# Kernel tuning notes

Measured on AMD Instinct MI355X. Metric: run time of the kernel, lower is better.

Reference implementation:

```python
import jax, jax.numpy as jnp
import numpy as np


def setup_inputs() -> dict:
    key = jax.random.key(0)
    ks = jax.random.split(key, 4)
    B, T, M, E, F = 4, 2048, 1024, 8, 4096
    hidden_states = jax.random.normal(ks[0], (B, T, M), dtype=jnp.float32)
    wg = jax.random.normal(ks[1], (M, E), dtype=jnp.float32) * (1.0 / np.sqrt(M))
    w1 = jax.random.normal(ks[2], (E, M, F), dtype=jnp.float32) * (1.0 / np.sqrt(M))
    b1 = jnp.zeros((E, F), dtype=jnp.float32)
    w2 = jax.random.normal(ks[3], (E, F, M), dtype=jnp.float32) * (1.0 / np.sqrt(F))
    b2 = jnp.zeros((E, M), dtype=jnp.float32)
    return {"hidden_states": hidden_states, "wg": wg, "w1": w1, "b1": b1, "w2": w2, "b2": b2}


def reference(hidden_states, wg, w1, b1, w2, b2):
    B, T, M = hidden_states.shape
    E = wg.shape[1]
    S = B * T
    MIN_CAPACITY = 4
    C = max((S + E - 1) // E, MIN_CAPACITY)  # capacity_factor = 1 (static)

    x = hidden_states.reshape(S, M)  # [S, M]

    # --- top-1 gating (deepspeed TopKGate, noisy=None, use_rts=False) ---
    logits = x @ wg                                  # [S, E]
    gates = jax.nn.softmax(logits, axis=-1)          # [S, E]
    idx = jnp.argmax(gates, axis=-1)                 # [S]
    mask1 = jax.nn.one_hot(idx, E, dtype=gates.dtype)  # [S, E]
    # aux loss (computed before capacity drop)
    l_aux = jnp.sum(gates.mean(0) * mask1.mean(0)) * E
    # position of each token within its expert's queue
    locations1 = jnp.cumsum(mask1, axis=0) - 1.0     # [S, E]
    mask1 = mask1 * (locations1 < C)                 # drop overflow tokens
    gates1_s = jnp.sum(gates * mask1, axis=1)        # [S]
    loc_s = jnp.sum(locations1 * mask1, axis=1).astype(jnp.int32)  # [S]
    loc_sc = jax.nn.one_hot(loc_s, C, dtype=gates.dtype)           # [S, C]

    combine_weights = jnp.einsum('se,sc->sec', gates1_s[:, None] * mask1, loc_sc)  # [S,E,C]
    dispatch_mask = (combine_weights > 0).astype(x.dtype)

    # --- dispatch ---
    dispatched = jnp.einsum('sec,sm->ecm', dispatch_mask, x)  # [E, C, M]

    # --- expert FFN (grouped GEMM) ---
    h = jax.nn.gelu(jnp.einsum('ecm,emf->ecf', dispatched, w1) + b1[:, None, :])
    expert_out = jnp.einsum('ecf,efm->ecm', h, w2) + b2[:, None, :]  # [E, C, M]

    # --- combine ---
    out = jnp.einsum('sec,ecm->sm', combine_weights, expert_out)  # [S, M]
    return out.reshape(B, T, M)
```

## Files before the change

kernel.cpp:

```cpp
#include <hip/hip_runtime.h>
#include <hip/hip_bf16.h>
#include <math.h>

#define S_TOK 8192
#define M_DIM 1024
#define E_NUM 8
#define F_DIM 4096
#define CAP   1024

typedef short short8 __attribute__((ext_vector_type(8)));
typedef float f32x4 __attribute__((ext_vector_type(4)));
typedef unsigned short ushortx4 __attribute__((ext_vector_type(4)));

__device__ inline unsigned short f2bf(float f) {
    union { float f; unsigned int u; } v; v.f = f;
    unsigned int r = v.u + 0x7fffu + ((v.u >> 16) & 1u);
    return (unsigned short)(r >> 16);
}

__device__ inline float gelu_fast(float x) {
    float y = 0.7978845608028654f * (x + 0.044715f * x * x * x);
    if (y > 40.f) return x;
    float e = exp2f(2.8853900817779268f * y);
    return x * e / (e + 1.0f);
}

__device__ inline void gl_lds16(const void* g, void* l) {
    __builtin_amdgcn_global_load_lds(
        (const __attribute__((address_space(1))) unsigned int*)g,
        (__attribute__((address_space(3))) unsigned int*)l, 16, 0, 0);
}

__global__ __launch_bounds__(256) void gating_kernel(
    const float* __restrict__ x, const float* __restrict__ wg,
    int* __restrict__ idx, float* __restrict__ gate)
{
    int wid = threadIdx.x >> 6;
    int lane = threadIdx.x & 63;
    int s = blockIdx.x * 4 + wid;
    const float* xs = x + (size_t)s * M_DIM;

    double acc[E_NUM];
#pragma unroll
    for (int e = 0; e < E_NUM; e++) acc[e] = 0.0;

    for (int i = lane; i < M_DIM; i += 64) {
        float xv = xs[i];
        float4 wa = *(const float4*)(wg + (size_t)i * E_NUM);
        float4 wb = *(const float4*)(wg + (size_t)i * E_NUM + 4);
        acc[0] += (double)xv * (double)wa.x;
        acc[1] += (double)xv * (double)wa.y;
        acc[2] += (double)xv * (double)wa.z;
        acc[3] += (double)xv * (double)wa.w;
        acc[4] += (double)xv * (double)wb.x;
        acc[5] += (double)xv * (double)wb.y;
        acc[6] += (double)xv * (double)wb.z;
        acc[7] += (double)xv * (double)wb.w;
    }
#pragma unroll
    for (int e = 0; e < E_NUM; e++) {
        double v = acc[e];
        for (int o = 32; o > 0; o >>= 1) v += __shfl_down(v, o, 64);
        acc[e] = v;
    }
    if (lane == 0) {
        double mx = acc[0]; int am = 0;
#pragma unroll
        for (int e = 1; e < E_NUM; e++) {
            if (acc[e] > mx) { mx = acc[e]; am = e; }
        }
        double se = 0.0;
#pragma unroll
        for (int e = 0; e < E_NUM; e++) se += exp(acc[e] - mx);
        idx[s] = am;
        gate[s] = (float)(1.0 / se);
    }
}

__global__ __launch_bounds__(1024) void scan_build(
    const int* __restrict__ idx, int* __restrict__ srcmap)
{
    __shared__ unsigned int sc[2][4][1024];
    int t = threadIdx.x;

    for (int i = t; i < E_NUM * CAP; i += 1024) srcmap[i] = -1;

    int eid[8];
    unsigned int cnt[E_NUM];
#pragma unroll
    for (int e = 0; e < E_NUM; e++) cnt[e] = 0;
#pragma unroll
    for (int i = 0; i < 8; i++) {
        int e = idx[t * 8 + i];
        eid[i] = e;
        cnt[e]++;
    }
    unsigned int pk[4];
#pragma unroll
    for (int i = 0; i < 4; i++) pk[i] = cnt[2 * i] | (cnt[2 * i + 1] << 16);
#pragma unroll
    for (int i = 0; i < 4; i++) sc[0][i][t] = pk[i];

    int buf = 0;
    for (int ofs = 1; ofs < 1024; ofs <<= 1) {
        __syncthreads();
        unsigned int v[4];
#pragma unroll
        for (int i = 0; i < 4; i++) {
            v[i] = sc[buf][i][t] + ((t >= ofs) ? sc[buf][i][t - ofs] : 0u);
            sc[buf ^ 1][i][t] = v[i];
        }
        buf ^= 1;
    }
    __syncthreads();
    unsigned int pos[E_NUM];
#pragma unroll
    for (int e = 0; e < E_NUM; e++) {
        unsigned int incl = (sc[buf][e >> 1][t] >> ((e & 1) * 16)) & 0xffffu;
        pos[e] = incl - cnt[e];
    }
#pragma unroll
    for (int i = 0; i < 8; i++) {
        int e = eid[i];
        unsigned int p = pos[e]++;
        if (p < CAP) srcmap[e * CAP + p] = t * 8 + i;
    }
}

__global__ __launch_bounds__(256) void dispatch_kernel(
    const float* __restrict__ x, const int* __restrict__ srcmap,
    unsigned short* __restrict__ A1)
{
    int slot = blockIdx.x;
    int s = srcmap[slot];
    int t = threadIdx.x;
    ushortx4 o;
    if (s >= 0) {
        float4 v = ((const float4*)(x + (size_t)s * M_DIM))[t];
        o[0] = f2bf(v.x); o[1] = f2bf(v.y); o[2] = f2bf(v.z); o[3] = f2bf(v.w);
    } else {
        o[0] = 0; o[1] = 0; o[2] = 0; o[3] = 0;
    }
    ((ushortx4*)(A1 + (size_t)slot * M_DIM))[t] = o;
}

__global__ __launch_bounds__(256) void transpose_cvt(
    const float* __restrict__ in, unsigned short* __restrict__ out, int R, int Cc)
{
    __shared__ float tile[32][33];
    int e = blockIdx.z;
    int br = blockIdx.y * 32, bc = blockIdx.x * 32;
    const float* ine = in + (size_t)e * R * Cc;
    unsigned short* oute = out + (size_t)e * R * Cc;
    int tx = threadIdx.x, ty = threadIdx.y;
#pragma unroll
    for (int i = 0; i < 32; i += 8)
        tile[ty + i][tx] = ine[(size_t)(br + ty + i) * Cc + (bc + tx)];
    __syncthreads();
#pragma unroll
    for (int i = 0; i < 32; i += 8)
        oute[(size_t)(bc + ty + i) * R + (br + tx)] = f2bf(tile[tx][ty + i]);
}

template <int MODE>
__global__ __launch_bounds__(512, 4) void gemm256x128(
    const unsigned short* __restrict__ A, const unsigned short* __restrict__ B,
    const float* __restrict__ bias, unsigned short* __restrict__ OutH,
    float* __restrict__ OutP)
{
    constexpr int K    = (MODE == 0) ? 1024 : 4096;
    constexpr int NB   = (MODE == 0) ? 4096 : 1024;
    constexpr int KLEN = (MODE == 0) ? 1024 : 2048;
    constexpr int NT   = KLEN / 32;
    constexpr int NWG  = (MODE == 0) ? 1024 : 512;
    constexpr int SLOT = 12288;

    __shared__ __align__(16) unsigned short LDS[3 * SLOT];

    int bid = blockIdx.x;
    int swz = (bid & 7) * (NWG / 8) + (bid >> 3);
    int e, tm, tn, ks;
    if (MODE == 0) {
        e = swz >> 7; int r = swz & 127; tn = r >> 2; tm = r & 3; ks = 0;
    } else {
        e = swz >> 6; int r = swz & 63; ks = r >> 5; int rr = r & 31;
        tn = rr >> 2; tm = rr & 3;
    }
    int kOff = (MODE == 0) ? 0 : ks * 2048;

    const unsigned short* Ae = A + ((size_t)e * CAP + (size_t)tm * 256) * K + kOff;
    const unsigned short* Be = B + ((size_t)e * NB + (size_t)tn * 128) * K + kOff;

    int tid = threadIdx.x, w = tid >> 6, lane = tid & 63;
    int wm = w >> 1, wn = w & 1;
    int fr = lane & 15, kq = lane >> 4;
    int r0 = wm * 64, c0 = wn * 64;

    int lr2 = lane >> 2, sl4 = lane & 3;
    int lc = sl4 ^ (lr2 & 3);
    const unsigned short* gA0 = Ae + (size_t)(w * 16 + lr2) * K + lc * 8;
    const unsigned short* gA1 = Ae + (size_t)(128 + w * 16 + lr2) * K + lc * 8;
    const unsigned short* gB  = Be + (size_t)(w * 16 + lr2) * K + lc * 8;
    int dA0 = (w * 16) * 32;
    int dA1 = (128 + w * 16) * 32;
    int dB  = 8192 + (w * 16) * 32;

#define STAGE(sl, t_) do { int ko_ = (t_) * 32;                      \
    gl_lds16(gA0 + ko_, &LDS[(sl) * SLOT + dA0]);                    \
    gl_lds16(gA1 + ko_, &LDS[(sl) * SLOT + dA1]);                    \
    gl_lds16(gB  + ko_, &LDS[(sl) * SLOT + dB]);                     \
} while (0)

    int swc = ((kq ^ (fr & 3)) << 3);
    int aoff = (r0 + fr) * 32 + swc;
    int boff = 8192 + (c0 + fr) * 32 + swc;

    f32x4 acc[4][4];
#pragma unroll
    for (int i = 0; i < 4; i++)
#pragma unroll
        for (int j = 0; j < 4; j++) acc[i][j] = (f32x4){0.f, 0.f, 0.f, 0.f};

    STAGE(0, 0);
    STAGE(1, 1);
    asm volatile("s_waitcnt vmcnt(3)" ::: "memory");
    __builtin_amdgcn_s_barrier();

    int cur = 0, stg = 2;
#pragma unroll 1
    for (int t = 0; t < NT; ++t) {
        if (t + 2 < NT) STAGE(stg, t + 2);

        int sb = cur * SLOT;
        short8 a[4], b[4];
#pragma unroll
        for (int mi = 0; mi < 4; mi++)
            a[mi] = *(const short8*)&LDS[sb + aoff + mi * 512];
#pragma unroll
        for (int ni = 0; ni < 4; ni++)
            b[ni] = *(const short8*)&LDS[sb + boff + ni * 512];
        __builtin_amdgcn_s_setprio(1);
#pragma unroll
        for (int mi = 0; mi < 4; mi++)
#pragma unroll
            for (int ni = 0; ni < 4; ni++)
                acc[mi][ni] = __builtin_amdgcn_mfma_f32_16x16x32_bf16(
                    a[mi], b[ni], acc[mi][ni], 0, 0, 0);
        __builtin_amdgcn_s_setprio(0);

        if (t + 2 < NT)      asm volatile("s_waitcnt vmcnt(3)" ::: "memory");
        else if (t + 1 < NT) asm volatile("s_waitcnt vmcnt(0)" ::: "memory");
        __builtin_amdgcn_s_barrier();
        cur = (cur + 1 == 3) ? 0 : cur + 1;
        stg = (stg + 1 == 3) ? 0 : stg + 1;
    }
#undef STAGE

    if (MODE == 0) {
        unsigned short* R = (unsigned short*)LDS;
        float bv[4];
#pragma unroll
        for (int ni = 0; ni < 4; ni++)
            bv[ni] = bias[e * NB + tn * 128 + c0 + ni * 16 + fr];
#pragma unroll
        for (int mi = 0; mi < 4; mi++) {
#pragma unroll
            for (int j = 0; j < 4; j++) {
                int row = wm * 64 + mi * 16 + kq * 4 + j;
#pragma unroll
                for (int ni = 0; ni < 4; ni++) {
                    int col = c0 + ni * 16 + fr;
                    R[row * 128 + (((col >> 3) ^ (row & 7)) << 3) + (col & 7)] =
                        f2bf(gelu_fast(acc[mi][ni][j] + bv[ni]));
                }
            }
        }
        __syncthreads();
        int row = tid >> 1, seg = tid & 1;
        size_t gb = ((size_t)(e * CAP + tm * 256 + row)) * NB + tn * 128 + seg * 64;
#pragma unroll
        for (int i = 0; i < 8; i++) {
            int chunk = seg * 8 + i;
            *(short8*)&OutH[gb + i * 8] =
                *(const short8*)&R[row * 128 + ((chunk ^ (row & 7)) << 3)];
        }
    } else {
        float* OP = OutP + (size_t)ks * S_TOK * M_DIM;
#pragma unroll
        for (int mi = 0; mi < 4; mi++) {
#pragma unroll
            for (int j = 0; j < 4; j++) {
                int r = tm * 256 + wm * 64 + mi * 16 + kq * 4 + j;
                size_t rowbase = ((size_t)(e * CAP + r)) * NB + tn * 128 + c0;
#pragma unroll
                for (int ni = 0; ni < 4; ni++)
                    OP[rowbase + ni * 16 + fr] = acc[mi][ni][j];
            }
        }
    }
}

__global__ __launch_bounds__(256) void combine_kernel(
    const float* __restrict__ P, const int* __restrict__ srcmap,
    const float* __restrict__ gate, const float* __restrict__ b2,
    float* __restrict__ out)
{
    int r = blockIdx.x;
    int s = srcmap[r];
    if (s < 0) return;
    int e = r >> 10;
    float g = gate[s];
    int t = threadIdx.x;
    float4 p0 = ((const float4*)P)[r * 256 + t];
    float4 p1 = ((const float4*)(P + (size_t)S_TOK * M_DIM))[r * 256 + t];
    float4 bb = ((const float4*)b2)[e * 256 + t];
    float4 o;
    o.x = g * (p0.x + p1.x + bb.x);
    o.y = g * (p0.y + p1.y + bb.y);
    o.z = g * (p0.z + p1.z + bb.z);
    o.w = g * (p0.w + p1.w + bb.w);
    ((float4*)out)[s * 256 + t] = o;
}

extern "C" void kernel_launch(void* const* d_in, const int* in_sizes, int n_in,
                              void* d_out, int out_size, void* d_ws, size_t ws_size,
                              hipStream_t stream) {
    const float* x  = (const float*)d_in[0];
    const float* wg = (const float*)d_in[1];
    const float* w1 = (const float*)d_in[2];
    const float* b1 = (const float*)d_in[3];
    const float* w2 = (const float*)d_in[4];
    const float* b2 = (const float*)d_in[5];
    float* out = (float*)d_out;

    char* ws = (char*)d_ws;
    unsigned short* A1  = (unsigned short*)(ws);
    unsigned short* W1T = (unsigned short*)(ws + (size_t)(16u << 20));
    float*          P   = (float*)(ws + (size_t)(16u << 20));
    unsigned short* W2T = (unsigned short*)(ws + (size_t)(80u << 20));
    unsigned short* H   = (unsigned short*)(ws + (size_t)(144u << 20));
    int*   idx  = (int*)(ws + (size_t)(208u << 20));
    float* gate = (float*)(ws + (size_t)(208u << 20) + 32768);
    int*   srcm = (int*)(ws + (size_t)(208u << 20) + 65536);

    hipMemsetAsync(d_out, 0, (size_t)S_TOK * M_DIM * sizeof(float), stream);

    gating_kernel<<<S_TOK / 4, 256, 0, stream>>>(x, wg, idx, gate);
    scan_build<<<1, 1024, 0, stream>>>(idx, srcm);
    dispatch_kernel<<<E_NUM * CAP, 256, 0, stream>>>(x, srcm, A1);
    transpose_cvt<<<dim3(F_DIM / 32, M_DIM / 32, E_NUM), dim3(32, 8), 0, stream>>>(
        w1, W1T, M_DIM, F_DIM);
    transpose_cvt<<<dim3(M_DIM / 32, F_DIM / 32, E_NUM), dim3(32, 8), 0, stream>>>(
        w2, W2T, F_DIM, M_DIM);

    gemm256x128<0><<<1024, 512, 0, stream>>>(A1, W1T, b1, H, nullptr);

    gemm256x128<1><<<512, 512, 0, stream>>>(H, W2T, nullptr, nullptr, P);

    combine_kernel<<<E_NUM * CAP, 256, 0, stream>>>(P, srcm, gate, b2, out);
}
```

Measured before the change: 336.4 us.

## Enlarge GEMM tiles to 256x256 with 1024-thread workgroups

Both expert GEMMs move from 256x128 tiles with 512 threads to 256x256 tiles with 16 waves per workgroup, laid out as 4x4 waves. Workgroup counts are halved and each thread now issues two async global-to-LDS loads per stage instead of three. The epilogue writes the bf16 tile through LDS in two 128-row halves so it fits the staging buffer. The aim is to raise arithmetic intensity and reduce global traffic per FLOP, at the cost of one workgroup per CU, fewer workgroups (256 for the second GEMM), and more LDS per workgroup.

```diff
diff --git a/kernel.cpp b/kernel.cpp
--- a/kernel.cpp
+++ b/kernel.cpp
@@ -163,7 +163,7 @@
 }
 
 template <int MODE>
-__global__ __launch_bounds__(512, 4) void gemm256x128(
+__global__ __launch_bounds__(1024, 1) void gemm256sq(
     const unsigned short* __restrict__ A, const unsigned short* __restrict__ B,
     const float* __restrict__ bias, unsigned short* __restrict__ OutH,
     float* __restrict__ OutP)
@@ -172,8 +172,8 @@
     constexpr int NB   = (MODE == 0) ? 4096 : 1024;
     constexpr int KLEN = (MODE == 0) ? 1024 : 2048;
     constexpr int NT   = KLEN / 32;
-    constexpr int NWG  = (MODE == 0) ? 1024 : 512;
-    constexpr int SLOT = 12288;
+    constexpr int NWG  = (MODE == 0) ? 512 : 256;
+    constexpr int SLOT = 16384;
 
     __shared__ __align__(16) unsigned short LDS[3 * SLOT];
 
@@ -181,39 +181,35 @@
     int swz = (bid & 7) * (NWG / 8) + (bid >> 3);
     int e, tm, tn, ks;
     if (MODE == 0) {
-        e = swz >> 7; int r = swz & 127; tn = r >> 2; tm = r & 3; ks = 0;
+        e = swz >> 6; int r = swz & 63; tn = r >> 2; tm = r & 3; ks = 0;
     } else {
-        e = swz >> 6; int r = swz & 63; ks = r >> 5; int rr = r & 31;
-        tn = rr >> 2; tm = rr & 3;
+        e = swz >> 5; int r = swz & 31; ks = r >> 4; int rr = r & 15;
+        tm = rr >> 2; tn = rr & 3;
     }
     int kOff = (MODE == 0) ? 0 : ks * 2048;
 
     const unsigned short* Ae = A + ((size_t)e * CAP + (size_t)tm * 256) * K + kOff;
-    const unsigned short* Be = B + ((size_t)e * NB + (size_t)tn * 128) * K + kOff;
+    const unsigned short* Be = B + ((size_t)e * NB + (size_t)tn * 256) * K + kOff;
 
     int tid = threadIdx.x, w = tid >> 6, lane = tid & 63;
-    int wm = w >> 1, wn = w & 1;
+    int wm = w >> 2, wn = w & 3;
     int fr = lane & 15, kq = lane >> 4;
-    int r0 = wm * 64, c0 = wn * 64;
 
     int lr2 = lane >> 2, sl4 = lane & 3;
     int lc = sl4 ^ (lr2 & 3);
-    const unsigned short* gA0 = Ae + (size_t)(w * 16 + lr2) * K + lc * 8;
-    const unsigned short* gA1 = Ae + (size_t)(128 + w * 16 + lr2) * K + lc * 8;
-    const unsigned short* gB  = Be + (size_t)(w * 16 + lr2) * K + lc * 8;
-    int dA0 = (w * 16) * 32;
-    int dA1 = (128 + w * 16) * 32;
-    int dB  = 8192 + (w * 16) * 32;
+    const unsigned short* gA = Ae + (size_t)(w * 16 + lr2) * K + lc * 8;
+    const unsigned short* gB = Be + (size_t)(w * 16 + lr2) * K + lc * 8;
+    int dA = (w * 16) * 32;
+    int dB = 8192 + (w * 16) * 32;
 
 #define STAGE(sl, t_) do { int ko_ = (t_) * 32;                      \
-    gl_lds16(gA0 + ko_, &LDS[(sl) * SLOT + dA0]);                    \
-    gl_lds16(gA1 + ko_, &LDS[(sl) * SLOT + dA1]);                    \
-    gl_lds16(gB  + ko_, &LDS[(sl) * SLOT + dB]);                     \
+    gl_lds16(gA + ko_, &LDS[(sl) * SLOT + dA]);                      \
+    gl_lds16(gB + ko_, &LDS[(sl) * SLOT + dB]);                      \
 } while (0)
 
     int swc = ((kq ^ (fr & 3)) << 3);
-    int aoff = (r0 + fr) * 32 + swc;
-    int boff = 8192 + (c0 + fr) * 32 + swc;
+    int aoff = (wm * 64 + fr) * 32 + swc;
+    int boff = 8192 + (wn * 64 + fr) * 32 + swc;
 
     f32x4 acc[4][4];
 #pragma unroll
@@ -223,7 +219,7 @@
 
     STAGE(0, 0);
     STAGE(1, 1);
-    asm volatile("s_waitcnt vmcnt(3)" ::: "memory");
+    asm volatile("s_waitcnt vmcnt(2)" ::: "memory");
     __builtin_amdgcn_s_barrier();
 
     int cur = 0, stg = 2;
@@ -248,7 +244,7 @@
                     a[mi], b[ni], acc[mi][ni], 0, 0, 0);
         __builtin_amdgcn_s_setprio(0);
 
-        if (t + 2 < NT)      asm volatile("s_waitcnt vmcnt(3)" ::: "memory");
+        if (t + 2 < NT)      asm volatile("s_waitcnt vmcnt(2)" ::: "memory");
         else if (t + 1 < NT) asm volatile("s_waitcnt vmcnt(0)" ::: "memory");
         __builtin_amdgcn_s_barrier();
         cur = (cur + 1 == 3) ? 0 : cur + 1;
@@ -261,28 +257,35 @@
         float bv[4];
 #pragma unroll
         for (int ni = 0; ni < 4; ni++)
-            bv[ni] = bias[e * NB + tn * 128 + c0 + ni * 16 + fr];
-#pragma unroll
-        for (int mi = 0; mi < 4; mi++) {
-#pragma unroll
-            for (int j = 0; j < 4; j++) {
-                int row = wm * 64 + mi * 16 + kq * 4 + j;
-#pragma unroll
-                for (int ni = 0; ni < 4; ni++) {
-                    int col = c0 + ni * 16 + fr;
-                    R[row * 128 + (((col >> 3) ^ (row & 7)) << 3) + (col & 7)] =
-                        f2bf(gelu_fast(acc[mi][ni][j] + bv[ni]));
+            bv[ni] = bias[e * NB + tn * 256 + wn * 64 + ni * 16 + fr];
+#pragma unroll 1
+        for (int h = 0; h < 2; ++h) {
+            __syncthreads();
+            if ((wm >> 1) == h) {
+#pragma unroll
+                for (int mi = 0; mi < 4; mi++) {
+#pragma unroll
+                    for (int j = 0; j < 4; j++) {
+                        int row = (wm & 1) * 64 + mi * 16 + kq * 4 + j;
+#pragma unroll
+                        for (int ni = 0; ni < 4; ni++) {
+                            int col = wn * 64 + ni * 16 + fr;
+                            R[row * 256 + (((col >> 3) ^ (row & 7)) << 3) + (col & 7)] =
+                                f2bf(gelu_fast(acc[mi][ni][j] + bv[ni]));
+                        }
+                    }
                 }
             }
-        }
-        __syncthreads();
-        int row = tid >> 1, seg = tid & 1;
-        size_t gb = ((size_t)(e * CAP + tm * 256 + row)) * NB + tn * 128 + seg * 64;
-#pragma unroll
-        for (int i = 0; i < 8; i++) {
-            int chunk = seg * 8 + i;
-            *(short8*)&OutH[gb + i * 8] =
-                *(const short8*)&R[row * 128 + ((chunk ^ (row & 7)) << 3)];
+            __syncthreads();
+            int row = tid >> 3, seg = tid & 7;
+            size_t gb = ((size_t)(e * CAP + tm * 256 + h * 128 + row)) * NB
+                        + tn * 256 + seg * 32;
+#pragma unroll
+            for (int i = 0; i < 4; i++) {
+                int chunk = seg * 4 + i;
+                *(short8*)&OutH[gb + i * 8] =
+                    *(const short8*)&R[row * 256 + ((chunk ^ (row & 7)) << 3)];
+            }
         }
     } else {
         float* OP = OutP + (size_t)ks * S_TOK * M_DIM;
@@ -291,7 +294,7 @@
 #pragma unroll
             for (int j = 0; j < 4; j++) {
                 int r = tm * 256 + wm * 64 + mi * 16 + kq * 4 + j;
-                size_t rowbase = ((size_t)(e * CAP + r)) * NB + tn * 128 + c0;
+                size_t rowbase = ((size_t)(e * CAP + r)) * NB + tn * 256 + wn * 64;
 #pragma unroll
                 for (int ni = 0; ni < 4; ni++)
                     OP[rowbase + ni * 16 + fr] = acc[mi][ni][j];
@@ -353,9 +356,9 @@
     transpose_cvt<<<dim3(M_DIM / 32, F_DIM / 32, E_NUM), dim3(32, 8), 0, stream>>>(
         w2, W2T, F_DIM, M_DIM);
 
-    gemm256x128<0><<<1024, 512, 0, stream>>>(A1, W1T, b1, H, nullptr);
-
-    gemm256x128<1><<<512, 512, 0, stream>>>(H, W2T, nullptr, nullptr, P);
+    gemm256sq<0><<<512, 1024, 0, stream>>>(A1, W1T, b1, H, nullptr);
+
+    gemm256sq<1><<<256, 1024, 0, stream>>>(H, W2T, nullptr, nullptr, P);
 
     combine_kernel<<<E_NUM * CAP, 256, 0, stream>>>(P, srcm, gate, b2, out);
 }
```

Measured after the change: 381.1 us. +13.3%, slower.
